# Performance work log

Measured on AMD Instinct MI355X. Metric: run time of the kernel, lower is better.

Reference implementation:

```python
import jax, jax.numpy as jnp
import numpy as np

B, N_ANG, LX, LY, LZ = 2, 120, 128, 128, 128


def _rotate_z(vol, phi):
    """Rotate vol [B,Lx,Ly,Lz] by phi radians (counterclockwise) in the (x,y)
    plane about the grid center, bilinear interpolation, zero padding.
    Mirrors pytomography's rotate_detector_z (bilinear grid-sample rotate)."""
    Lx, Ly = vol.shape[1], vol.shape[2]
    dt = vol.dtype
    cx = (Lx - 1) / 2.0
    cy = (Ly - 1) / 2.0
    xs = jnp.arange(Lx, dtype=dt) - cx
    ys = jnp.arange(Ly, dtype=dt) - cy
    X, Y = jnp.meshgrid(xs, ys, indexing="ij")  # [Lx,Ly]
    c, s = jnp.cos(phi), jnp.sin(phi)
    # inverse rotation maps each output pixel to its source location
    sx = c * X + s * Y + cx
    sy = -s * X + c * Y + cy
    x0 = jnp.floor(sx)
    y0 = jnp.floor(sy)
    wx = (sx - x0)[None, :, :, None]
    wy = (sy - y0)[None, :, :, None]
    x0i = x0.astype(jnp.int32)
    y0i = y0.astype(jnp.int32)

    def gather(xi, yi):
        valid = (xi >= 0) & (xi < Lx) & (yi >= 0) & (yi < Ly)
        xic = jnp.clip(xi, 0, Lx - 1)
        yic = jnp.clip(yi, 0, Ly - 1)
        v = vol[:, xic, yic, :]  # [B,Lx,Ly,Lz]
        return v * valid.astype(dt)[None, :, :, None]

    v00 = gather(x0i, y0i)
    v01 = gather(x0i, y0i + 1)
    v10 = gather(x0i + 1, y0i)
    v11 = gather(x0i + 1, y0i + 1)
    return (v00 * (1 - wx) * (1 - wy) + v01 * (1 - wx) * wy
            + v10 * wx * (1 - wy) + v11 * wx * wy)


def setup_inputs() -> dict:
    key = jax.random.key(0)
    image = jax.random.uniform(key, (B, N_ANG, LY, LZ), dtype=jnp.float32)
    angles = jnp.linspace(0.0, 360.0, N_ANG, endpoint=False).astype(jnp.float32)
    return {"image": image, "angles": angles}


def reference(image, angles, delta=1e-11):
    # image: [B, N_angles, Lr, Lz]; angles in degrees.
    Bn, Na, Lr, Lz = image.shape
    Lx = Ly = Lr
    dt = image.dtype
    phis = -jnp.deg2rad(angles).astype(dt)  # negative=True -> back-rotation

    def step(carry, inp):
        obj_acc, norm_acc = carry
        proj, phi = inp  # proj: [B, Lr, Lz]
        # image[:, i].unsqueeze(1) * ones([B, Lx, Ly, Lz]): broadcast along x
        obj_i = jnp.broadcast_to(proj[:, None, :, :], (Bn, Lx, Ly, Lz))
        norm_i = jnp.ones((Bn, Lx, Ly, Lz), dt)
        obj_acc = obj_acc + _rotate_z(obj_i, phi)
        norm_acc = norm_acc + _rotate_z(norm_i, phi)
        return (obj_acc, norm_acc), None

    init = (jnp.zeros((Bn, Lx, Ly, Lz), dt), jnp.zeros((Bn, Lx, Ly, Lz), dt))
    (obj, norm), _ = jax.lax.scan(step, init, (jnp.swapaxes(image, 0, 1), phis))
    return obj / (norm + jnp.asarray(delta, dt))
```

## Files before the change

### kernel.cpp

```cpp
#include <hip/hip_runtime.h>

namespace {

constexpr int L     = 128;
constexpr int NANG  = 120;
constexpr int NPTS  = 16;
constexpr size_t H16_BYTES = (size_t)2 * NANG * L * L * 2;

typedef __fp16 f16x2 __attribute__((ext_vector_type(2)));
typedef __fp16 f16x4 __attribute__((ext_vector_type(4)));
typedef float  f32x4 __attribute__((ext_vector_type(4)));

__global__ __launch_bounds__(256) void cvt16_kernel(const float* __restrict__ in,
                                                    unsigned* __restrict__ out) {
    const int i = ((int)blockIdx.x * 256 + (int)threadIdx.x) * 4;
    const float4 v = *reinterpret_cast<const float4*>(in + i);
    f16x2 a = __builtin_amdgcn_cvt_pkrtz(v.x, v.y);
    f16x2 b = __builtin_amdgcn_cvt_pkrtz(v.z, v.w);
    uint2 st;
    st.x = *reinterpret_cast<unsigned*>(&a);
    st.y = *reinterpret_cast<unsigned*>(&b);
    *reinterpret_cast<uint2*>(out + i / 2) = st;
}

template <bool F16>
__global__ __launch_bounds__(512, 8) void bp_kernel(
    const void* __restrict__ imgv,
    const float* __restrict__ angles,
    float* __restrict__ out)
{
    constexpr unsigned SLICE = F16 ? 32768u : 65536u;
    constexpr unsigned ROWB  = F16 ? 256u  : 512u;
    constexpr int      RSH   = F16 ? 8 : 9;

    __shared__ alignas(16) unsigned long long aftab[NANG * 2 * NPTS];
    __shared__ float2   acs[NANG];
    __shared__ unsigned arloB[NANG];
    __shared__ alignas(16) float nrmtab[NPTS];

    const int tid = threadIdx.x;
    const int bid = (int)blockIdx.x;
    const int n   = ((bid & 7) << 7) | (bid >> 3);
    int xt = 0, yt = 0;
#pragma unroll
    for (int i = 0; i < 5; ++i) {
        xt |= ((n >> (2 * i)) & 1) << i;
        yt |= ((n >> (2 * i + 1)) & 1) << i;
    }
    const int xb = xt * 4, yb = yt * 4;
    const float cx = (L - 1) * 0.5f;

    if (tid < NANG) {
        const float phi = -angles[tid] * 0.017453292519943295f;
        float s, c;
        sincosf(phi, &s, &c);
        const float X0 = (float)xb - cx,  X1 = (float)(xb + 3) - cx;
        const float Y0 = (float)yb - cx,  Y1 = (float)(yb + 3) - cx;
        const float a00 = -s * X0 + c * Y0 + cx;
        const float a01 = -s * X0 + c * Y1 + cx;
        const float a10 = -s * X1 + c * Y0 + cx;
        const float a11 = -s * X1 + c * Y1 + cx;
        const float symin = fminf(fminf(a00, a01), fminf(a10, a11));
        acs[tid]   = make_float2(c, s);
        arloB[tid] = (unsigned)min(max((int)floorf(symin) - 1, 0), 120) << RSH;
    }
    if (tid < NPTS) nrmtab[tid] = 0.f;
    __syncthreads();

    float wsum = 0.f;
#pragma unroll
    for (int k = 0; k < 4; ++k) {
        const int e = tid + k * 512;
        if (e < NANG * NPTS) {
            const int p = e & 15;
            const int a = e >> 4;
            const float2 cs = acs[a];
            const int rlo = (int)(arloB[a] >> RSH);
            const float X = (float)(xb + (p >> 2)) - cx;
            const float Y = (float)(yb + (p & 3)) - cx;
            const float sx =  cs.x * X + cs.y * Y + cx;
            const float sy = -cs.y * X + cs.x * Y + cx;
            const float x0f = floorf(sx), y0f = floorf(sy);
            const float wx = sx - x0f,    wy = sy - y0f;
            const int x0 = (int)x0f, y0 = (int)y0f;
            const float mx0 = (x0 >= 0  && x0 <  L)     ? 1.f : 0.f;
            const float mx1 = (x0 >= -1 && x0 <= L - 2) ? 1.f : 0.f;
            const float my0 = (y0 >= 0  && y0 <  L)     ? 1.f : 0.f;
            const float my1 = (y0 >= -1 && y0 <= L - 2) ? 1.f : 0.f;
            const float A   = (1.f - wx) * mx0 + wx * mx1;
            float w0f = (1.f - wy) * my0 * A;
            float w1f = wy * my1 * A;
            const int y0c = min(max(y0, 0), L - 1);
            const int y1c = min(max(y0 + 1, 0), L - 1);
            const int s0  = min(max(y0c - rlo, 0), 7);
            const int s1  = min(max(y1c - rlo, 0), 7);
            if (s0 == s1) { w0f += w1f; w1f = 0.f; }
            f16x2 wh = __builtin_amdgcn_cvt_pkrtz(w0f, w1f);
            const unsigned wbits = *reinterpret_cast<unsigned*>(&wh);
            const unsigned t  = (unsigned)s0 & 3u;
            const int      q0 = s0 >> 2;
            const unsigned long long W = (unsigned long long)wbits << (t * 16u);
            const unsigned long long spill =
                (t == 3u) ? (unsigned long long)(wbits >> 16) : 0ull;
            aftab[a * 32 + p]      = (q0 == 0) ? W : 0ull;
            aftab[a * 32 + 16 + p] = (q0 == 1) ? W : spill;
            wsum += w0f + w1f;
        }
    }
    atomicAdd(&nrmtab[tid & 15], wsum);
    __syncthreads();

    const int wave  = tid >> 6;
    const int lane  = tid & 63;
    const int quad  = lane >> 4;
    const int lhalf = lane & 15;
    const int sel   = quad >> 1;
    const int lq    = quad & 1;
    const int b     = wave & 1;
    const int zh    = (wave >> 1) & 1;
    const int aset  = wave >> 2;
    const char* __restrict__ imgc = (const char*)imgv;

    const unsigned bbase_s = __builtin_amdgcn_readfirstlane((unsigned)(b * NANG) * SLICE);
    const unsigned voffc = (unsigned)sel * SLICE
                         + (unsigned)(lq * 4) * ROWB
                         + (unsigned)(zh * 64 + 4 * lhalf) * (F16 ? 2u : 4u);
    const int p0 = aset * 30;

    f32x4 acc[4] = {};

    auto issue = [&](uint2* r, float4* rfp, unsigned long long& afs, int i) {
        const int pr = p0 + i;
        afs = aftab[pr * 64 + lane];
        const unsigned rlB = arloB[2 * pr + sel];
        const char* pa = imgc + (bbase_s + (unsigned)(2 * pr) * SLICE);
        const unsigned voff = voffc + rlB;
        if constexpr (F16) {
#pragma unroll
            for (int j = 0; j < 4; ++j)
                r[j] = *(const uint2*)(pa + (voff + (unsigned)j * ROWB));
        } else {
#pragma unroll
            for (int j = 0; j < 4; ++j)
                rfp[j] = *(const float4*)(pa + (voff + (unsigned)j * ROWB));
        }
    };
    auto compute = [&](const uint2* r, const float4* rfp, unsigned long long afu) {
        union { unsigned long long u; f16x4 v; } c; c.u = afu;
        f16x4 bf[4];
        if constexpr (F16) {
            union { unsigned u[2]; f16x4 v; } t;
            t.u[0] = __builtin_amdgcn_perm(r[1].x, r[0].x, 0x05040100u);
            t.u[1] = __builtin_amdgcn_perm(r[3].x, r[2].x, 0x05040100u);
            bf[0] = t.v;
            t.u[0] = __builtin_amdgcn_perm(r[1].x, r[0].x, 0x07060302u);
            t.u[1] = __builtin_amdgcn_perm(r[3].x, r[2].x, 0x07060302u);
            bf[1] = t.v;
            t.u[0] = __builtin_amdgcn_perm(r[1].y, r[0].y, 0x05040100u);
            t.u[1] = __builtin_amdgcn_perm(r[3].y, r[2].y, 0x05040100u);
            bf[2] = t.v;
            t.u[0] = __builtin_amdgcn_perm(r[1].y, r[0].y, 0x07060302u);
            t.u[1] = __builtin_amdgcn_perm(r[3].y, r[2].y, 0x07060302u);
            bf[3] = t.v;
        } else {
#pragma unroll
            for (int k = 0; k < 4; ++k) {
                const f16x2 ha = __builtin_amdgcn_cvt_pkrtz(rfp[0][k], rfp[1][k]);
                const f16x2 hb = __builtin_amdgcn_cvt_pkrtz(rfp[2][k], rfp[3][k]);
                bf[k] = f16x4{ha.x, ha.y, hb.x, hb.y};
            }
        }
#pragma unroll
        for (int k = 0; k < 4; ++k)
            acc[k] = __builtin_amdgcn_mfma_f32_16x16x16f16(c.v, bf[k], acc[k], 0, 0, 0);
    };

    uint2  ru0[4], ru1[4], ru2[4];
    float4 rf0[4], rf1[4], rf2[4];
    unsigned long long af0, af1, af2;

    issue(ru0, rf0, af0, 0);
    issue(ru1, rf1, af1, 1);

    for (int i = 0; i < 30; i += 3) {
        if (i + 2 < 30) issue(ru2, rf2, af2, i + 2);
        compute(ru0, rf0, af0);
        if (i + 3 < 30) issue(ru0, rf0, af0, i + 3);
        compute(ru1, rf1, af1);
        if (i + 4 < 30) issue(ru1, rf1, af1, i + 4);
        compute(ru2, rf2, af2);
    }

    __syncthreads();
    float4* red = reinterpret_cast<float4*>(aftab);
    if (aset == 1) {
#pragma unroll
        for (int k = 0; k < 4; ++k)
            red[k * 256 + (wave & 3) * 64 + lane] = *(const float4*)&acc[k];
    }
    __syncthreads();
    if (aset == 0) {
#pragma unroll
        for (int k = 0; k < 4; ++k) {
            const float4 o = red[k * 256 + (wave & 3) * 64 + lane];
            acc[k][0] += o.x; acc[k][1] += o.y; acc[k][2] += o.z; acc[k][3] += o.w;
        }
        const float4 nrm4 = *(const float4*)&nrmtab[quad * 4];
        const float iv[4] = { 1.f / (nrm4.x + 1e-11f), 1.f / (nrm4.y + 1e-11f),
                              1.f / (nrm4.z + 1e-11f), 1.f / (nrm4.w + 1e-11f) };
        const int zb = zh * 64 + 4 * lhalf;
#pragma unroll
        for (int r = 0; r < 4; ++r) {
            const int pnt = quad * 4 + r;
            const int x = xb + (pnt >> 2);
            const int y = yb + (pnt & 3);
            const float4 o = make_float4(acc[0][r] * iv[r], acc[1][r] * iv[r],
                                         acc[2][r] * iv[r], acc[3][r] * iv[r]);
            *reinterpret_cast<float4*>(&out[(((size_t)(b * L + x)) * L + y) * L + zb]) = o;
        }
    }
}

}

extern "C" void kernel_launch(void* const* d_in, const int* in_sizes, int n_in,
                              void* d_out, int out_size, void* d_ws, size_t ws_size,
                              hipStream_t stream) {
    const float* image  = (const float*)d_in[0];
    const float* angles = (const float*)d_in[1];
    float* out = (float*)d_out;
    (void)in_sizes; (void)n_in; (void)out_size;

    dim3 grid(1024);
    if (d_ws != nullptr && ws_size >= H16_BYTES) {
        cvt16_kernel<<<dim3(3840), 256, 0, stream>>>(image, (unsigned*)d_ws);
        bp_kernel<true><<<grid, 512, 0, stream>>>(d_ws, angles, out);
    } else {
        bp_kernel<false><<<grid, 512, 0, stream>>>(image, angles, out);
    }
}
```

Measured before the change: 104.8 us.

## Enlarge xy tile to 8x8 per block with 1024 threads and four angle groups

Measured after the change: 108.2 us. +3.2%, slower.

```diff
diff --git a/kernel.cpp b/kernel.cpp
--- a/kernel.cpp
+++ b/kernel.cpp
@@ -4,7 +4,6 @@
 
 constexpr int L     = 128;
 constexpr int NANG  = 120;
-constexpr int NPTS  = 16;
 constexpr size_t H16_BYTES = (size_t)2 * NANG * L * L * 2;
 
 typedef __fp16 f16x2 __attribute__((ext_vector_type(2)));
@@ -24,7 +23,7 @@
 }
 
 template <bool F16>
-__global__ __launch_bounds__(512, 8) void bp_kernel(
+__global__ __launch_bounds__(1024, 4) void bp_kernel(
     const void* __restrict__ imgv,
     const float* __restrict__ angles,
     float* __restrict__ out)
@@ -33,51 +32,53 @@
     constexpr unsigned ROWB  = F16 ? 256u  : 512u;
     constexpr int      RSH   = F16 ? 8 : 9;
 
-    __shared__ alignas(16) unsigned long long aftab[NANG * 2 * NPTS];
+    __shared__ uint4    wtab[NANG * 64];
     __shared__ float2   acs[NANG];
     __shared__ unsigned arloB[NANG];
-    __shared__ alignas(16) float nrmtab[NPTS];
+    __shared__ alignas(16) float nrmtab[64];
 
     const int tid = threadIdx.x;
     const int bid = (int)blockIdx.x;
-    const int n   = ((bid & 7) << 7) | (bid >> 3);
+    const int n   = ((bid & 7) << 6) | (bid >> 3);
+    const int b   = n & 1;
+    const int tt  = n >> 1;
     int xt = 0, yt = 0;
 #pragma unroll
-    for (int i = 0; i < 5; ++i) {
-        xt |= ((n >> (2 * i)) & 1) << i;
-        yt |= ((n >> (2 * i + 1)) & 1) << i;
-    }
-    const int xb = xt * 4, yb = yt * 4;
+    for (int i = 0; i < 4; ++i) {
+        xt |= ((tt >> (2 * i)) & 1) << i;
+        yt |= ((tt >> (2 * i + 1)) & 1) << i;
+    }
+    const int xb = xt * 8, yb = yt * 8;
     const float cx = (L - 1) * 0.5f;
 
     if (tid < NANG) {
         const float phi = -angles[tid] * 0.017453292519943295f;
         float s, c;
         sincosf(phi, &s, &c);
-        const float X0 = (float)xb - cx,  X1 = (float)(xb + 3) - cx;
-        const float Y0 = (float)yb - cx,  Y1 = (float)(yb + 3) - cx;
+        const float X0 = (float)xb - cx,  X1 = (float)(xb + 7) - cx;
+        const float Y0 = (float)yb - cx,  Y1 = (float)(yb + 7) - cx;
         const float a00 = -s * X0 + c * Y0 + cx;
         const float a01 = -s * X0 + c * Y1 + cx;
         const float a10 = -s * X1 + c * Y0 + cx;
         const float a11 = -s * X1 + c * Y1 + cx;
         const float symin = fminf(fminf(a00, a01), fminf(a10, a11));
         acs[tid]   = make_float2(c, s);
-        arloB[tid] = (unsigned)min(max((int)floorf(symin) - 1, 0), 120) << RSH;
-    }
-    if (tid < NPTS) nrmtab[tid] = 0.f;
+        arloB[tid] = (unsigned)min(max((int)floorf(symin), 0), 116) << RSH;
+    }
+    if (tid < 64) nrmtab[tid] = 0.f;
     __syncthreads();
 
     float wsum = 0.f;
 #pragma unroll
-    for (int k = 0; k < 4; ++k) {
-        const int e = tid + k * 512;
-        if (e < NANG * NPTS) {
-            const int p = e & 15;
-            const int a = e >> 4;
+    for (int k = 0; k < 8; ++k) {
+        const int e = tid + k * 1024;
+        if (e < NANG * 64) {
+            const int p = e & 63;
+            const int a = e >> 6;
             const float2 cs = acs[a];
             const int rlo = (int)(arloB[a] >> RSH);
-            const float X = (float)(xb + (p >> 2)) - cx;
-            const float Y = (float)(yb + (p & 3)) - cx;
+            const float X = (float)(xb + (p >> 3)) - cx;
+            const float Y = (float)(yb + (p & 7)) - cx;
             const float sx =  cs.x * X + cs.y * Y + cx;
             const float sy = -cs.y * X + cs.x * Y + cx;
             const float x0f = floorf(sx), y0f = floorf(sy);
@@ -92,131 +93,140 @@
             float w1f = wy * my1 * A;
             const int y0c = min(max(y0, 0), L - 1);
             const int y1c = min(max(y0 + 1, 0), L - 1);
-            const int s0  = min(max(y0c - rlo, 0), 7);
-            const int s1  = min(max(y1c - rlo, 0), 7);
+            const int s0  = min(max(y0c - rlo, 0), 11);
+            const int s1  = min(max(y1c - rlo, 0), 11);
             if (s0 == s1) { w0f += w1f; w1f = 0.f; }
             f16x2 wh = __builtin_amdgcn_cvt_pkrtz(w0f, w1f);
             const unsigned wbits = *reinterpret_cast<unsigned*>(&wh);
             const unsigned t  = (unsigned)s0 & 3u;
-            const int      q0 = s0 >> 2;
+            const unsigned q0 = (unsigned)s0 >> 2;
             const unsigned long long W = (unsigned long long)wbits << (t * 16u);
-            const unsigned long long spill =
-                (t == 3u) ? (unsigned long long)(wbits >> 16) : 0ull;
-            aftab[a * 32 + p]      = (q0 == 0) ? W : 0ull;
-            aftab[a * 32 + 16 + p] = (q0 == 1) ? W : spill;
+            const unsigned spill = (t == 3u) ? (wbits >> 16) : 0u;
+            uint4 ent;
+            ent.x = (unsigned)W;
+            ent.y = (unsigned)(W >> 32);
+            ent.z = spill;
+            ent.w = q0;
+            wtab[a * 64 + p] = ent;
             wsum += w0f + w1f;
         }
     }
-    atomicAdd(&nrmtab[tid & 15], wsum);
+    atomicAdd(&nrmtab[tid & 63], wsum);
     __syncthreads();
 
     const int wave  = tid >> 6;
     const int lane  = tid & 63;
     const int quad  = lane >> 4;
     const int lhalf = lane & 15;
-    const int sel   = quad >> 1;
-    const int lq    = quad & 1;
-    const int b     = wave & 1;
-    const int zh    = (wave >> 1) & 1;
+    const int zq    = wave & 3;
     const int aset  = wave >> 2;
     const char* __restrict__ imgc = (const char*)imgv;
 
-    const unsigned bbase_s = __builtin_amdgcn_readfirstlane((unsigned)(b * NANG) * SLICE);
-    const unsigned voffc = (unsigned)sel * SLICE
-                         + (unsigned)(lq * 4) * ROWB
-                         + (unsigned)(zh * 64 + 4 * lhalf) * (F16 ? 2u : 4u);
-    const int p0 = aset * 30;
-
-    f32x4 acc[4] = {};
-
-    auto issue = [&](uint2* r, float4* rfp, unsigned long long& afs, int i) {
-        const int pr = p0 + i;
-        afs = aftab[pr * 64 + lane];
-        const unsigned rlB = arloB[2 * pr + sel];
-        const char* pa = imgc + (bbase_s + (unsigned)(2 * pr) * SLICE);
-        const unsigned voff = voffc + rlB;
+    const unsigned bbase_s = (unsigned)(b * NANG) * SLICE;
+    const unsigned voffc = (unsigned)((quad == 3) ? 0 : quad) * 4u * ROWB
+                         + (unsigned)(zq * 32 + 2 * lhalf) * (F16 ? 2u : 4u);
+    const int a0 = aset * 30;
+
+    f32x4 acc[4][2] = {};
+
+    auto issue = [&](uint4* e, unsigned* r, float2* rf, int i) {
+        const int a = a0 + i;
+#pragma unroll
+        for (int m = 0; m < 4; ++m)
+            e[m] = wtab[a * 64 + m * 16 + lhalf];
+        const unsigned rlB = __builtin_amdgcn_readfirstlane(arloB[a]);
+        const char* pa = imgc + (bbase_s + (unsigned)a * SLICE + rlB);
         if constexpr (F16) {
 #pragma unroll
             for (int j = 0; j < 4; ++j)
-                r[j] = *(const uint2*)(pa + (voff + (unsigned)j * ROWB));
+                r[j] = *(const unsigned*)(pa + (voffc + (unsigned)j * ROWB));
         } else {
 #pragma unroll
             for (int j = 0; j < 4; ++j)
-                rfp[j] = *(const float4*)(pa + (voff + (unsigned)j * ROWB));
+                rf[j] = *(const float2*)(pa + (voffc + (unsigned)j * ROWB));
         }
     };
-    auto compute = [&](const uint2* r, const float4* rfp, unsigned long long afu) {
-        union { unsigned long long u; f16x4 v; } c; c.u = afu;
-        f16x4 bf[4];
+    auto compute = [&](const uint4* e, const unsigned* r, const float2* rf) {
+        union { unsigned u[2]; f16x4 v; } B0, B1;
         if constexpr (F16) {
-            union { unsigned u[2]; f16x4 v; } t;
-            t.u[0] = __builtin_amdgcn_perm(r[1].x, r[0].x, 0x05040100u);
-            t.u[1] = __builtin_amdgcn_perm(r[3].x, r[2].x, 0x05040100u);
-            bf[0] = t.v;
-            t.u[0] = __builtin_amdgcn_perm(r[1].x, r[0].x, 0x07060302u);
-            t.u[1] = __builtin_amdgcn_perm(r[3].x, r[2].x, 0x07060302u);
-            bf[1] = t.v;
-            t.u[0] = __builtin_amdgcn_perm(r[1].y, r[0].y, 0x05040100u);
-            t.u[1] = __builtin_amdgcn_perm(r[3].y, r[2].y, 0x05040100u);
-            bf[2] = t.v;
-            t.u[0] = __builtin_amdgcn_perm(r[1].y, r[0].y, 0x07060302u);
-            t.u[1] = __builtin_amdgcn_perm(r[3].y, r[2].y, 0x07060302u);
-            bf[3] = t.v;
+            B0.u[0] = __builtin_amdgcn_perm(r[1], r[0], 0x05040100u);
+            B0.u[1] = __builtin_amdgcn_perm(r[3], r[2], 0x05040100u);
+            B1.u[0] = __builtin_amdgcn_perm(r[1], r[0], 0x07060302u);
+            B1.u[1] = __builtin_amdgcn_perm(r[3], r[2], 0x07060302u);
         } else {
-#pragma unroll
-            for (int k = 0; k < 4; ++k) {
-                const f16x2 ha = __builtin_amdgcn_cvt_pkrtz(rfp[0][k], rfp[1][k]);
-                const f16x2 hb = __builtin_amdgcn_cvt_pkrtz(rfp[2][k], rfp[3][k]);
-                bf[k] = f16x4{ha.x, ha.y, hb.x, hb.y};
+            const f16x2 h0a = __builtin_amdgcn_cvt_pkrtz(rf[0].x, rf[1].x);
+            const f16x2 h0b = __builtin_amdgcn_cvt_pkrtz(rf[2].x, rf[3].x);
+            const f16x2 h1a = __builtin_amdgcn_cvt_pkrtz(rf[0].y, rf[1].y);
+            const f16x2 h1b = __builtin_amdgcn_cvt_pkrtz(rf[2].y, rf[3].y);
+            B0.v = f16x4{h0a.x, h0a.y, h0b.x, h0b.y};
+            B1.v = f16x4{h1a.x, h1a.y, h1b.x, h1b.y};
+        }
+#pragma unroll
+        for (int m = 0; m < 4; ++m) {
+            const int q0 = (int)e[m].w;
+            union { unsigned u[2]; f16x4 v; } af;
+            af.u[0] = (quad == q0) ? e[m].x : ((quad == q0 + 1) ? e[m].z : 0u);
+            af.u[1] = (quad == q0) ? e[m].y : 0u;
+            acc[m][0] = __builtin_amdgcn_mfma_f32_16x16x16f16(af.v, B0.v, acc[m][0], 0, 0, 0);
+            acc[m][1] = __builtin_amdgcn_mfma_f32_16x16x16f16(af.v, B1.v, acc[m][1], 0, 0, 0);
+        }
+    };
+
+    uint4    eA[4], eB[4], eC[4];
+    unsigned rA[4], rB[4], rC[4];
+    float2   fA[4], fB[4], fC[4];
+
+    issue(eA, rA, fA, 0);
+    issue(eB, rB, fB, 1);
+
+    for (int i = 0; i < 30; i += 3) {
+        if (i + 2 < 30) issue(eC, rC, fC, i + 2);
+        compute(eA, rA, fA);
+        if (i + 3 < 30) issue(eA, rA, fA, i + 3);
+        compute(eB, rB, fB);
+        if (i + 4 < 30) issue(eB, rB, fB, i + 4);
+        compute(eC, rC, fC);
+    }
+
+    __syncthreads();
+    float4* red = reinterpret_cast<float4*>(wtab);
+    if (aset > 0) {
+#pragma unroll
+        for (int m = 0; m < 4; ++m)
+#pragma unroll
+            for (int zg = 0; zg < 2; ++zg)
+                red[(((aset - 1) * 4 + zq) * 8 + m * 2 + zg) * 64 + lane] =
+                    make_float4(acc[m][zg][0], acc[m][zg][1],
+                                acc[m][zg][2], acc[m][zg][3]);
+    }
+    __syncthreads();
+    if (aset == 0) {
+#pragma unroll
+        for (int s = 0; s < 3; ++s)
+#pragma unroll
+            for (int m = 0; m < 4; ++m)
+#pragma unroll
+                for (int zg = 0; zg < 2; ++zg) {
+                    const float4 o = red[((s * 4 + zq) * 8 + m * 2 + zg) * 64 + lane];
+                    acc[m][zg][0] += o.x; acc[m][zg][1] += o.y;
+                    acc[m][zg][2] += o.z; acc[m][zg][3] += o.w;
+                }
+        const int zb = zq * 32 + 2 * lhalf;
+#pragma unroll
+        for (int m = 0; m < 4; ++m) {
+            const float4 nrm4 = *(const float4*)&nrmtab[m * 16 + quad * 4];
+            const float iv[4] = { 1.f / (nrm4.x + 1e-11f), 1.f / (nrm4.y + 1e-11f),
+                                  1.f / (nrm4.z + 1e-11f), 1.f / (nrm4.w + 1e-11f) };
+#pragma unroll
+            for (int r = 0; r < 4; ++r) {
+                const int p = m * 16 + quad * 4 + r;
+                const int x = xb + (p >> 3);
+                const int y = yb + (p & 7);
+                const float2 o = make_float2(acc[m][0][r] * iv[r],
+                                             acc[m][1][r] * iv[r]);
+                *reinterpret_cast<float2*>(
+                    &out[(((size_t)(b * L + x)) * L + y) * L + zb]) = o;
             }
-        }
-#pragma unroll
-        for (int k = 0; k < 4; ++k)
-            acc[k] = __builtin_amdgcn_mfma_f32_16x16x16f16(c.v, bf[k], acc[k], 0, 0, 0);
-    };
-
-    uint2  ru0[4], ru1[4], ru2[4];
-    float4 rf0[4], rf1[4], rf2[4];
-    unsigned long long af0, af1, af2;
-
-    issue(ru0, rf0, af0, 0);
-    issue(ru1, rf1, af1, 1);
-
-    for (int i = 0; i < 30; i += 3) {
-        if (i + 2 < 30) issue(ru2, rf2, af2, i + 2);
-        compute(ru0, rf0, af0);
-        if (i + 3 < 30) issue(ru0, rf0, af0, i + 3);
-        compute(ru1, rf1, af1);
-        if (i + 4 < 30) issue(ru1, rf1, af1, i + 4);
-        compute(ru2, rf2, af2);
-    }
-
-    __syncthreads();
-    float4* red = reinterpret_cast<float4*>(aftab);
-    if (aset == 1) {
-#pragma unroll
-        for (int k = 0; k < 4; ++k)
-            red[k * 256 + (wave & 3) * 64 + lane] = *(const float4*)&acc[k];
-    }
-    __syncthreads();
-    if (aset == 0) {
-#pragma unroll
-        for (int k = 0; k < 4; ++k) {
-            const float4 o = red[k * 256 + (wave & 3) * 64 + lane];
-            acc[k][0] += o.x; acc[k][1] += o.y; acc[k][2] += o.z; acc[k][3] += o.w;
-        }
-        const float4 nrm4 = *(const float4*)&nrmtab[quad * 4];
-        const float iv[4] = { 1.f / (nrm4.x + 1e-11f), 1.f / (nrm4.y + 1e-11f),
-                              1.f / (nrm4.z + 1e-11f), 1.f / (nrm4.w + 1e-11f) };
-        const int zb = zh * 64 + 4 * lhalf;
-#pragma unroll
-        for (int r = 0; r < 4; ++r) {
-            const int pnt = quad * 4 + r;
-            const int x = xb + (pnt >> 2);
-            const int y = yb + (pnt & 3);
-            const float4 o = make_float4(acc[0][r] * iv[r], acc[1][r] * iv[r],
-                                         acc[2][r] * iv[r], acc[3][r] * iv[r]);
-            *reinterpret_cast<float4*>(&out[(((size_t)(b * L + x)) * L + y) * L + zb]) = o;
         }
     }
 }
@@ -231,11 +241,11 @@
     float* out = (float*)d_out;
     (void)in_sizes; (void)n_in; (void)out_size;
 
-    dim3 grid(1024);
+    dim3 grid(512);
     if (d_ws != nullptr && ws_size >= H16_BYTES) {
         cvt16_kernel<<<dim3(3840), 256, 0, stream>>>(image, (unsigned*)d_ws);
-        bp_kernel<true><<<grid, 512, 0, stream>>>(d_ws, angles, out);
+        bp_kernel<true><<<grid, 1024, 0, stream>>>(d_ws, angles, out);
     } else {
-        bp_kernel<false><<<grid, 512, 0, stream>>>(image, angles, out);
-    }
-}
+        bp_kernel<false><<<grid, 1024, 0, stream>>>(image, angles, out);
+    }
+}
```
